# Kernel tuning notes

Hardware: AMD Instinct MI355X
Metric: run time of the kernel (lower is better)

Reference implementation:

```python
import jax, jax.numpy as jnp
import numpy as np

N_NODES = 50000
N_EDGES = 500000
D = 128  # input_dim == output_dim -> residual is identity


def _linear(x, W, b):
    return x @ W + b


def setup_inputs() -> dict:
    rng = np.random.default_rng(0)
    ei = rng.integers(0, N_NODES, size=(2, N_EDGES))
    # one-time structure cache: unique (src,dst) pairs + multiplicity counts
    pairs = np.stack([ei[0], ei[1]], axis=1)
    uniq, counts = np.unique(pairs, axis=0, return_counts=True)

    key = jax.random.key(0)
    ks = jax.random.split(key, 16)
    s = 0.02
    inp = {
        "x": jax.random.normal(ks[0], (N_NODES, D), jnp.float32),
        "src": jnp.asarray(uniq[:, 0], jnp.int32),
        "dst": jnp.asarray(uniq[:, 1], jnp.int32),
        "counts": jnp.asarray(counts, jnp.float32),
        # lin_src_to_dst / lin_dst_to_src (stored as [in, out])
        "W_sd": jax.random.normal(ks[1], (D, D), jnp.float32) * s,
        "b_sd": jnp.zeros((D,), jnp.float32),
        "W_ds": jax.random.normal(ks[2], (D, D), jnp.float32) * s,
        "b_ds": jnp.zeros((D,), jnp.float32),
        # lcs_mlp: Linear(2D, D) -> ReLU -> Linear(D, 1)
        "W_l1": jax.random.normal(ks[3], (2 * D, D), jnp.float32) * s,
        "b_l1": jnp.zeros((D,), jnp.float32),
        "W_l2": jax.random.normal(ks[4], (D, 1), jnp.float32) * s,
        "b_l2": jnp.zeros((1,), jnp.float32),
        # gate_mlp: Linear(2D, D) -> ReLU -> Linear(D, 1)
        "W_g1": jax.random.normal(ks[5], (2 * D, D), jnp.float32) * s,
        "b_g1": jnp.zeros((D,), jnp.float32),
        "W_g2": jax.random.normal(ks[6], (D, 1), jnp.float32) * s,
        "b_g2": jnp.zeros((1,), jnp.float32),
    }
    return inp


def reference(x, src, dst, counts, W_sd, b_sd, W_ds, b_ds,
              W_l1, b_l1, W_l2, b_l2, W_g1, b_g1, W_g2, b_g2):
    num_nodes = x.shape[0]
    x_src = x[src]                      # [E, D] gather
    x_dst = x[dst]                      # [E, D] gather

    # LCS score per unique edge (computed under no_grad in torch -> stop_gradient)
    lcs_in = jnp.concatenate([x_src, x_dst], axis=-1)           # [E, 2D]
    h = jax.nn.relu(_linear(lcs_in, W_l1, b_l1))
    lcs = jax.nn.sigmoid(_linear(h, W_l2, b_l2))                # [E, 1]
    lcs = jax.lax.stop_gradient(lcs)

    cnt = counts[:, None]                                       # [E, 1]
    msg_in = _linear(x_src, W_sd, b_sd) * lcs * cnt             # [E, D]
    msg_out = _linear(x_dst, W_ds, b_ds) * lcs * cnt            # [E, D]

    h_in = jax.ops.segment_sum(msg_in, dst, num_segments=num_nodes)
    h_out = jax.ops.segment_sum(msg_out, src, num_segments=num_nodes)

    in_deg = jnp.clip(jax.ops.segment_sum(counts, dst, num_segments=num_nodes), 1.0)
    out_deg = jnp.clip(jax.ops.segment_sum(counts, src, num_segments=num_nodes), 1.0)
    h_in = h_in / in_deg[:, None]
    h_out = h_out / out_deg[:, None]

    gate_in = jnp.concatenate([h_in, h_out], axis=-1)           # [N, 2D]
    g = jax.nn.relu(_linear(gate_in, W_g1, b_g1))
    gate = jax.nn.sigmoid(_linear(g, W_g2, b_g2))               # [N, 1]

    fused = gate * h_in + (1.0 - gate) * h_out
    return fused + x  # residual is Identity (input_dim == output_dim)
```

## Files before the change

### kernel.cpp

```cpp
#include <hip/hip_runtime.h>
#include <math.h>

typedef unsigned int uint;
typedef unsigned long long ull;

#define THREADS 256
#define NC 96

typedef __attribute__((ext_vector_type(8))) short bf16x8;
typedef __attribute__((ext_vector_type(4))) float f32x4;

__device__ __forceinline__ float blo(uint u) { return __uint_as_float(u << 16); }
__device__ __forceinline__ float bhi(uint u) { return __uint_as_float(u & 0xffff0000u); }
__device__ __forceinline__ uint  bf16r(float x) {
    uint u = __float_as_uint(x);
    return (u + 0x7fffu + ((u >> 16) & 1u)) >> 16;
}
__device__ __forceinline__ uint packbf(float lo, float hi) {
    return bf16r(lo) | (bf16r(hi) << 16);
}

__global__ __launch_bounds__(THREADS)
void transpose_w(const float* __restrict__ W_sd, const float* __restrict__ W_ds,
                 const float* __restrict__ W_l1, const float* __restrict__ W_g1,
                 ushort* __restrict__ Wt, ushort* __restrict__ Wtg1)
{
    __shared__ float tile[32][33];
    const int y = blockIdx.y;
    const float* src;
    ushort* dst;
    int dstK, kofs;
    if (y < 4) {
        src = (y == 0) ? W_sd : (y == 1) ? W_ds : (y == 2) ? W_l1 : (W_l1 + 16384);
        dst = Wt + y * 16384; dstK = 128; kofs = 0;
    } else {
        src = W_g1 + (y - 4) * 16384;
        dst = Wtg1; dstK = 256; kofs = (y - 4) * 128;
    }
    const int tix = blockIdx.x;
    const int k0 = (tix & 3) * 32, n0 = (tix >> 2) * 32;
    const int t = threadIdx.x;

    {
        const int r = t >> 3, c8 = t & 7;
        const float4 f = *(const float4*)(src + (size_t)(k0 + r) * 128 + n0 + c8 * 4);
        tile[r][c8 * 4 + 0] = f.x; tile[r][c8 * 4 + 1] = f.y;
        tile[r][c8 * 4 + 2] = f.z; tile[r][c8 * 4 + 3] = f.w;
    }
    __syncthreads();
    {
        const int n = t >> 3, k8 = t & 7;
        const float v0 = tile[k8 * 4 + 0][n], v1 = tile[k8 * 4 + 1][n];
        const float v2 = tile[k8 * 4 + 2][n], v3 = tile[k8 * 4 + 3][n];
        uint2 o; o.x = packbf(v0, v1); o.y = packbf(v2, v3);
        *(uint2*)(dst + (size_t)(n0 + n) * dstK + kofs + k0 + k8 * 4) = o;
    }
}

__device__ __forceinline__ void mfma_tile_compute(const char* AsB, const char* BtB,
                                                  int wv, int ln, f32x4 acc[8])
{
    const int mrow = wv * 16 + (ln & 15);
    const int kgb  = (ln >> 4) * 16;
#pragma unroll
    for (int kk = 0; kk < 4; ++kk) {
        const int kbyte = kk * 64 + kgb;
        const bf16x8 a = *(const bf16x8*)(AsB + mrow * 256 + (kbyte ^ ((mrow & 7) << 4)));
#pragma unroll
        for (int tt = 0; tt < 8; ++tt) {
            const int nrow = tt * 16 + (ln & 15);
            const bf16x8 b = *(const bf16x8*)(BtB + nrow * 256 + (kbyte ^ ((nrow & 7) << 4)));
            acc[tt] = __builtin_amdgcn_mfma_f32_16x16x32_bf16(a, b, acc[tt], 0, 0, 0);
        }
    }
}

__global__ __launch_bounds__(THREADS)
void gemm_node_count(const float* __restrict__ X, int M,
                     const ushort* __restrict__ Wt,
                     const float* __restrict__ b_sd, const float* __restrict__ b_ds,
                     const float* __restrict__ b_l1,
                     ushort* __restrict__ Pb,
                     const int* __restrict__ src, const int* __restrict__ dst,
                     const float* __restrict__ counts,
                     ull* __restrict__ packed_in, int* __restrict__ off_out,
                     int E, int ST, int BPG)
{
    __shared__ __align__(16) char BtB[32768];
    __shared__ __align__(16) char AsB[17408];

    const int tid = threadIdx.x;
    const int bid = blockIdx.x;

    if (bid < NC) {
        const int stride = NC * THREADS;
        for (int e = bid * THREADS + tid; e < E; e += stride) {
            const int  d = dst[e];
            const uint c = (uint)counts[e];
            atomicAdd(packed_in + d, (1ULL << 32) | (ull)c);
        }
        for (int e = bid * THREADS + tid; e < E; e += stride) {
            const int cur  = src[e];
            const int prev = (e == 0) ? -1 : src[e - 1];
            for (int v = prev + 1; v <= cur; ++v) off_out[v] = e;
            if (e == E - 1)
                for (int v = cur + 1; v <= M; ++v) off_out[v] = E;
        }
        return;
    }

    const int q    = bid - NC;
    const int grp  = q & 3;
    const int sidx = q >> 2;
    const int wv = tid >> 6, ln = tid & 63;
    const int r = tid >> 2, seg = tid & 3;

    if (sidx * 4 >= ST) return;

    {
        const int rn = tid >> 1, sg = tid & 1;
        const uint4* ws = (const uint4*)(Wt + grp * 16384 + (size_t)rn * 128 + sg * 64);
#pragma unroll
        for (int i = 0; i < 8; ++i) {
            const uint4 u = ws[i];
            const int kbyte = sg * 128 + i * 16;
            *(uint4*)(BtB + rn * 256 + (kbyte ^ ((rn & 7) << 4))) = u;
        }
    }

    const float* bias = (grp == 0) ? b_sd : (grp == 1) ? b_ds
                      : (grp == 2) ? b_l1 : nullptr;
    float bv[8];
#pragma unroll
    for (int tt = 0; tt < 8; ++tt)
        bv[tt] = bias ? bias[tt * 16 + (ln & 15)] : 0.f;

    float4 fa[8];
    {
        int gr = sidx * 4 * 64 + r; if (gr >= M) gr = M - 1;
        const float4* xs = (const float4*)(X + (size_t)gr * 128 + seg * 32);
#pragma unroll
        for (int i = 0; i < 8; ++i) fa[i] = xs[i];
    }

    for (int k = 0; k < 4; ++k) {
        const int s = sidx * 4 + k;
        if (s >= ST) break;
        __syncthreads();

#pragma unroll
        for (int i = 0; i < 4; ++i) {
            const float4 f0 = fa[i * 2], f1 = fa[i * 2 + 1];
            uint4 u;
            u.x = packbf(f0.x, f0.y); u.y = packbf(f0.z, f0.w);
            u.z = packbf(f1.x, f1.y); u.w = packbf(f1.z, f1.w);
            const int kbyte = seg * 64 + i * 16;
            *(uint4*)(AsB + r * 256 + (kbyte ^ ((r & 7) << 4))) = u;
        }
        __syncthreads();

        if (k < 3 && s + 1 < ST) {
            int gr = (s + 1) * 64 + r; if (gr >= M) gr = M - 1;
            const float4* xs = (const float4*)(X + (size_t)gr * 128 + seg * 32);
#pragma unroll
            for (int i = 0; i < 8; ++i) fa[i] = xs[i];
        }

        f32x4 acc[8];
#pragma unroll
        for (int tt = 0; tt < 8; ++tt) acc[tt] = (f32x4){0.f, 0.f, 0.f, 0.f};
        mfma_tile_compute(AsB, BtB, wv, ln, acc);
        __syncthreads();

#pragma unroll
        for (int tt = 0; tt < 8; ++tt) {
            const int n = tt * 16 + (ln & 15);
#pragma unroll
            for (int r2 = 0; r2 < 4; ++r2) {
                const int m = wv * 16 + ((ln >> 4) << 2) + r2;
                ((ushort*)AsB)[m * 136 + n] = (ushort)bf16r(acc[tt][r2] + bv[tt]);
            }
        }
        __syncthreads();

        {
            const int gr = s * 64 + r;
            if (gr < M) {
                uint4* dstp = (uint4*)Pb + (size_t)gr * 64 + grp * 16 + seg * 4;
#pragma unroll
                for (int i = 0; i < 4; ++i)
                    dstp[i] = *(const uint4*)(AsB + r * 272 + (seg * 4 + i) * 16);
            }
        }
    }
}

__global__ __launch_bounds__(256)
void scan_p1(const ull* __restrict__ packed_in, int* __restrict__ bsum, int M)
{
    __shared__ int s[256];
    const int t = threadIdx.x;
    const int i = blockIdx.x * 256 + t;
    s[t] = (i < M) ? (int)(packed_in[i] >> 32) : 0;
    __syncthreads();
#pragma unroll
    for (int o = 128; o; o >>= 1) {
        if (t < o) s[t] += s[t + o];
        __syncthreads();
    }
    if (t == 0) bsum[blockIdx.x] = s[0];
}

__global__ __launch_bounds__(1024)
void scan_p2(int* __restrict__ bsum, int NB)
{
    __shared__ int s[1024];
    const int t = threadIdx.x;
    const int v = (t < NB) ? bsum[t] : 0;
    s[t] = v;
    __syncthreads();
    for (int o = 1; o < 1024; o <<= 1) {
        const int u = (t >= o) ? s[t - o] : 0;
        __syncthreads();
        s[t] += u;
        __syncthreads();
    }
    if (t < NB) bsum[t] = s[t] - v;
}

__global__ __launch_bounds__(256)
void scan_p3(const ull* __restrict__ packed_in, const int* __restrict__ bsum,
             int* __restrict__ off_in, int M)
{
    __shared__ int s[256];
    const int t = threadIdx.x;
    const int i = blockIdx.x * 256 + t;
    const int v = (i < M) ? (int)(packed_in[i] >> 32) : 0;
    s[t] = v;
    __syncthreads();
    for (int o = 1; o < 256; o <<= 1) {
        const int u = (t >= o) ? s[t - o] : 0;
        __syncthreads();
        s[t] += u;
        __syncthreads();
    }
    if (i < M) off_in[i] = bsum[blockIdx.x] + s[t] - v;
}

__global__ __launch_bounds__(THREADS)
void edge_out(const ushort* __restrict__ Pb, ushort* __restrict__ Hout,
              const int* __restrict__ dst, const float* __restrict__ counts,
              const float* __restrict__ W_l2, const float* __restrict__ b_l2,
              const int* __restrict__ off_out,
              const int* __restrict__ off_in, int* __restrict__ cur_in,
              float2* __restrict__ uw_in, int M)
{
    const int lane = threadIdx.x & 63;
    const int wid  = threadIdx.x >> 6;
    const int v    = blockIdx.x * 4 + wid;
    if (v >= M) return;
    const int g  = lane >> 4;
    const int gl = lane & 15;

    const uint* rs = (const uint*)Pb + (size_t)v * 256;
    const uint4 av = ((const uint4*)(rs + 128))[gl];
    const float4 wa = ((const float4*)W_l2)[gl * 2];
    const float4 wb = ((const float4*)W_l2)[gl * 2 + 1];
    const float bl2 = b_l2[0];

    const int base = off_out[v];
    const int end  = off_out[v + 1];

    float a0 = 0.f, a1 = 0.f, a2 = 0.f, a3 = 0.f;
    float a4 = 0.f, a5 = 0.f, a6 = 0.f, a7 = 0.f;
    float dg = 0.f;

    int j = base + g;
    int   d0 = 0;  float c0 = 0.f;
    uint4 bv0 = {0, 0, 0, 0}, pv0 = {0, 0, 0, 0};
    if (j < end) {
        d0 = dst[j]; c0 = counts[j];
        const uint* rd = (const uint*)Pb + (size_t)d0 * 256;
        bv0 = ((const uint4*)(rd + 192))[gl];
        pv0 = ((const uint4*)(rd + 64))[gl];
    }

    for (; j < end; j += 4) {
        const int jn = j + 4;
        const int jc = (jn < end) ? jn : j;
        const int   d1 = dst[jc];
        const float c1 = counts[jc];
        const uint* rdn = (const uint*)Pb + (size_t)d1 * 256;
        const uint4 bv1 = ((const uint4*)(rdn + 192))[gl];
        const uint4 pv1 = ((const uint4*)(rdn + 64))[gl];

        float part =
            fmaxf(blo(av.x) + blo(bv0.x), 0.f) * wa.x + fmaxf(bhi(av.x) + bhi(bv0.x), 0.f) * wa.y +
            fmaxf(blo(av.y) + blo(bv0.y), 0.f) * wa.z + fmaxf(bhi(av.y) + bhi(bv0.y), 0.f) * wa.w +
            fmaxf(blo(av.z) + blo(bv0.z), 0.f) * wb.x + fmaxf(bhi(av.z) + bhi(bv0.z), 0.f) * wb.y +
            fmaxf(blo(av.w) + blo(bv0.w), 0.f) * wb.z + fmaxf(bhi(av.w) + bhi(bv0.w), 0.f) * wb.w;
        part += __shfl_xor(part, 1);
        part += __shfl_xor(part, 2);
        part += __shfl_xor(part, 4);
        part += __shfl_xor(part, 8);

        const float w = c0 / (1.f + __expf(-(part + bl2)));

        a0 = fmaf(blo(pv0.x), w, a0); a1 = fmaf(bhi(pv0.x), w, a1);
        a2 = fmaf(blo(pv0.y), w, a2); a3 = fmaf(bhi(pv0.y), w, a3);
        a4 = fmaf(blo(pv0.z), w, a4); a5 = fmaf(bhi(pv0.z), w, a5);
        a6 = fmaf(blo(pv0.w), w, a6); a7 = fmaf(bhi(pv0.w), w, a7);
        dg += c0;

        if (gl == 0) {
            const int r1 = atomicAdd(cur_in + d0, 1);
            uw_in[off_in[d0] + r1] = make_float2(__int_as_float(v), w);
        }

        d0 = d1; c0 = c1; bv0 = bv1; pv0 = pv1;
    }

#define RED2(a) a += __shfl_xor(a, 16); a += __shfl_xor(a, 32);
    RED2(a0) RED2(a1) RED2(a2) RED2(a3) RED2(a4) RED2(a5) RED2(a6) RED2(a7) RED2(dg)
#undef RED2

    if (g == 0) {
        const float r = 1.f / fmaxf(dg, 1.f);
        uint4 o;
        o.x = packbf(a0 * r, a1 * r);
        o.y = packbf(a2 * r, a3 * r);
        o.z = packbf(a4 * r, a5 * r);
        o.w = packbf(a6 * r, a7 * r);
        ((uint4*)((uint*)Hout + (size_t)v * 64))[gl] = o;
    }
}

__global__ __launch_bounds__(THREADS)
void agg_in(ushort* __restrict__ Pb,
            const float2* __restrict__ uw_in,
            const int* __restrict__ off_in, const ull* __restrict__ packed_in,
            int M)
{
    const int lane = threadIdx.x & 63;
    const int wid  = threadIdx.x >> 6;
    const int v    = blockIdx.x * 4 + wid;
    if (v >= M) return;
    const int g  = lane >> 4;
    const int gl = lane & 15;

    const ull pk = packed_in[v];
    const int n  = (int)(pk >> 32);
    const float dg = (float)(uint)(pk & 0xffffffffu);
    const float2* __restrict__ uw = uw_in + off_in[v];

    float a0 = 0.f, a1 = 0.f, a2 = 0.f, a3 = 0.f;
    float a4 = 0.f, a5 = 0.f, a6 = 0.f, a7 = 0.f;

    int j = g;
    float2 p0 = make_float2(0.f, 0.f);
    uint4  pv0 = {0, 0, 0, 0};
    if (j < n) {
        p0 = uw[j];
        pv0 = ((const uint4*)((const uint*)Pb + (size_t)__float_as_int(p0.x) * 256))[gl];
    }

    for (; j < n; j += 4) {
        const int jn = j + 4;
        const int jc = (jn < n) ? jn : j;
        const float2 p1 = uw[jc];
        const uint4  pv1 = ((const uint4*)((const uint*)Pb + (size_t)__float_as_int(p1.x) * 256))[gl];

        const float w = p0.y;
        a0 = fmaf(blo(pv0.x), w, a0); a1 = fmaf(bhi(pv0.x), w, a1);
        a2 = fmaf(blo(pv0.y), w, a2); a3 = fmaf(bhi(pv0.y), w, a3);
        a4 = fmaf(blo(pv0.z), w, a4); a5 = fmaf(bhi(pv0.z), w, a5);
        a6 = fmaf(blo(pv0.w), w, a6); a7 = fmaf(bhi(pv0.w), w, a7);

        p0 = p1; pv0 = pv1;
    }
#define RED2(a) a += __shfl_xor(a, 16); a += __shfl_xor(a, 32);
    RED2(a0) RED2(a1) RED2(a2) RED2(a3) RED2(a4) RED2(a5) RED2(a6) RED2(a7)
#undef RED2

    if (g == 0) {
        const float r = 1.f / fmaxf(dg, 1.f);
        uint4 o;
        o.x = packbf(a0 * r, a1 * r);
        o.y = packbf(a2 * r, a3 * r);
        o.z = packbf(a4 * r, a5 * r);
        o.w = packbf(a6 * r, a7 * r);
        ((uint4*)((uint*)Pb + (size_t)v * 256 + 128))[gl] = o;
    }
}

__global__ __launch_bounds__(THREADS)
void gate_final(const ushort* __restrict__ Pb, const ushort* __restrict__ Hout,
                int M,
                const ushort* __restrict__ Wtg1, const float* __restrict__ b_g1,
                const float* __restrict__ W_g2, const float* __restrict__ b_g2,
                const float* __restrict__ x, float* __restrict__ out)
{
    __shared__ __align__(16) char AsB[16384];
    __shared__ __align__(16) char BtB[32768];

    const int tid = threadIdx.x;
    const int m0  = blockIdx.x * 64;
    const int wv = tid >> 6, ln = tid & 63;

    f32x4 acc[8];
#pragma unroll
    for (int tt = 0; tt < 8; ++tt) acc[tt] = (f32x4){0.f, 0.f, 0.f, 0.f};

    for (int h = 0; h < 2; ++h) {
        if (h) __syncthreads();
        {
            const int r = tid >> 2, seg = tid & 3;
            int gr = m0 + r; if (gr >= M) gr = M - 1;
            const uint4* ps = (h == 0)
                ? ((const uint4*)Pb + (size_t)gr * 64 + 32 + seg * 4)
                : ((const uint4*)Hout + (size_t)gr * 16 + seg * 4);
#pragma unroll
            for (int i = 0; i < 4; ++i) {
                const uint4 u = ps[i];
                const int kbyte = seg * 64 + i * 16;
                *(uint4*)(AsB + r * 256 + (kbyte ^ ((r & 7) << 4))) = u;
            }
        }
        {
            const int rn = tid >> 1, sg = tid & 1;
            const uint4* ws = (const uint4*)Wtg1 + (size_t)rn * 32 + h * 16 + sg * 8;
#pragma unroll
            for (int i = 0; i < 8; ++i) {
                const uint4 u = ws[i];
                const int kbyte = sg * 128 + i * 16;
                *(uint4*)(BtB + rn * 256 + (kbyte ^ ((rn & 7) << 4))) = u;
            }
        }
        __syncthreads();
        mfma_tile_compute(AsB, BtB, wv, ln, acc);
    }

    __syncthreads();
#pragma unroll
    for (int tt = 0; tt < 8; ++tt) {
        const int n = tt * 16 + (ln & 15);
        const float bv = b_g1[n];
#pragma unroll
        for (int r = 0; r < 4; ++r) {
            const int m = wv * 16 + ((ln >> 4) << 2) + r;
            const float val = fmaxf(acc[tt][r] + bv, 0.f);
            const float pr  = __shfl_xor(val, 1);
            if ((ln & 1) == 0)
                ((uint*)BtB)[m * 68 + (n >> 1)] = packbf(val, pr);
        }
    }
    __syncthreads();

    const float bg2 = b_g2[0];
    const float2 w2 = ((const float2*)W_g2)[ln];
#pragma unroll 4
    for (int r = 0; r < 16; ++r) {
        const int row = wv * 16 + r;
        const int gr  = m0 + row;
        const uint gv = ((const uint*)BtB)[row * 68 + ln];
        float part = blo(gv) * w2.x + bhi(gv) * w2.y;
#pragma unroll
        for (int off = 32; off; off >>= 1) part += __shfl_xor(part, off);
        const float gate = 1.f / (1.f + __expf(-(part + bg2)));
        if (gr < M) {
            const uint hin = ((const uint*)Pb)[(size_t)gr * 256 + 128 + ln];
            const uint hov = ((const uint*)Hout)[(size_t)gr * 64 + ln];
            const float2 xv = ((const float2*)x)[(size_t)gr * 64 + ln];
            float2 o;
            o.x = gate * blo(hin) + (1.f - gate) * blo(hov) + xv.x;
            o.y = gate * bhi(hin) + (1.f - gate) * bhi(hov) + xv.y;
            ((float2*)out)[(size_t)gr * 64 + ln] = o;
        }
    }
}

extern "C" void kernel_launch(void* const* d_in, const int* in_sizes, int n_in,
                              void* d_out, int out_size, void* d_ws, size_t ws_size,
                              hipStream_t stream)
{
    const float* x     = (const float*)d_in[0];
    const int*   src   = (const int*)  d_in[1];
    const int*   dst   = (const int*)  d_in[2];
    const float* cnts  = (const float*)d_in[3];
    const float* W_sd  = (const float*)d_in[4];
    const float* b_sd  = (const float*)d_in[5];
    const float* W_ds  = (const float*)d_in[6];
    const float* b_ds  = (const float*)d_in[7];
    const float* W_l1  = (const float*)d_in[8];
    const float* b_l1  = (const float*)d_in[9];
    const float* W_l2  = (const float*)d_in[10];
    const float* b_l2  = (const float*)d_in[11];
    const float* W_g1  = (const float*)d_in[12];
    const float* b_g1  = (const float*)d_in[13];
    const float* W_g2  = (const float*)d_in[14];
    const float* b_g2  = (const float*)d_in[15];

    const int M = in_sizes[0] / 128;
    const int E = in_sizes[1];

    ushort* Pb        = (ushort*)d_ws;
    ushort* Wt        = Pb + (size_t)M * 512;
    ushort* Wtg1      = Wt + 4 * 16384;
    ushort* Hout      = Wtg1 + 32768;
    ull*    packed_in = (ull*)(Hout + (size_t)M * 128);
    int*    cur_in    = (int*)(packed_in + M);
    float2* uw_in     = (float2*)(cur_in + M);
    int*    off_in    = (int*)(uw_in + E);
    int*    off_out   = off_in + M;
    int*    bsum      = off_out + M + 1;

    hipMemsetAsync(packed_in, 0, 12 * (size_t)M, stream);

    transpose_w<<<dim3(16, 6), THREADS, 0, stream>>>(W_sd, W_ds, W_l1, W_g1, Wt, Wtg1);

    const int ST  = (M + 63) / 64;
    const int BPG = (ST + 3) / 4;
    gemm_node_count<<<NC + 4 * BPG, THREADS, 0, stream>>>(
        x, M, Wt, b_sd, b_ds, b_l1, Pb, src, dst, cnts, packed_in, off_out,
        E, ST, BPG);

    const int NB = (M + 255) / 256;
    scan_p1<<<NB, 256, 0, stream>>>(packed_in, bsum, M);
    scan_p2<<<1, 1024, 0, stream>>>(bsum, NB);
    scan_p3<<<NB, 256, 0, stream>>>(packed_in, bsum, off_in, M);

    edge_out<<<(M + 3) / 4, THREADS, 0, stream>>>(
        Pb, Hout, dst, cnts, W_l2, b_l2, off_out, off_in, cur_in, uw_in, M);

    agg_in<<<(M + 3) / 4, THREADS, 0, stream>>>(Pb, uw_in, off_in, packed_in, M);

    gate_final<<<(M + 63) / 64, THREADS, 0, stream>>>(Pb, Hout, M, Wtg1, b_g1,
                                                      W_g2, b_g2, x, (float*)d_out);
}
```

Before: 182.2 us.

## Load GEMM A operand directly into registers and remap blocks across XCDs

The node GEMM now loads X rows straight into MFMA A-fragment registers instead of staging them through shared memory, which removes several barriers and the LDS A buffer. Results are written directly from accumulators as packed bf16 pairs via lane shuffles instead of an LDS transpose and coalesced uint4 stores. Block indices are also permuted so that consecutive work items are spread across the eight XCDs, with the grid padded to a multiple of 8. The trade is less LDS traffic and synchronisation against uncoalesced 4-byte global stores and strided global loads of X.

```diff
diff --git a/kernel.cpp b/kernel.cpp
--- a/kernel.cpp
+++ b/kernel.cpp
@@ -57,24 +57,6 @@
     }
 }
 
-__device__ __forceinline__ void mfma_tile_compute(const char* AsB, const char* BtB,
-                                                  int wv, int ln, f32x4 acc[8])
-{
-    const int mrow = wv * 16 + (ln & 15);
-    const int kgb  = (ln >> 4) * 16;
-#pragma unroll
-    for (int kk = 0; kk < 4; ++kk) {
-        const int kbyte = kk * 64 + kgb;
-        const bf16x8 a = *(const bf16x8*)(AsB + mrow * 256 + (kbyte ^ ((mrow & 7) << 4)));
-#pragma unroll
-        for (int tt = 0; tt < 8; ++tt) {
-            const int nrow = tt * 16 + (ln & 15);
-            const bf16x8 b = *(const bf16x8*)(BtB + nrow * 256 + (kbyte ^ ((nrow & 7) << 4)));
-            acc[tt] = __builtin_amdgcn_mfma_f32_16x16x32_bf16(a, b, acc[tt], 0, 0, 0);
-        }
-    }
-}
-
 __global__ __launch_bounds__(THREADS)
 void gemm_node_count(const float* __restrict__ X, int M,
                      const ushort* __restrict__ Wt,
@@ -84,10 +66,9 @@
                      const int* __restrict__ src, const int* __restrict__ dst,
                      const float* __restrict__ counts,
                      ull* __restrict__ packed_in, int* __restrict__ off_out,
-                     int E, int ST, int BPG)
+                     int E, int ST, int NG)
 {
     __shared__ __align__(16) char BtB[32768];
-    __shared__ __align__(16) char AsB[17408];
 
     const int tid = threadIdx.x;
     const int bid = blockIdx.x;
@@ -109,13 +90,15 @@
         return;
     }
 
-    const int q    = bid - NC;
-    const int grp  = q & 3;
-    const int sidx = q >> 2;
+    const int bg   = bid - NC;
+    const int per  = NG >> 3;
+    const int p    = (bg & 7) * per + (bg >> 3);
+    if (p >= NG) return;
+    const int grp  = p & 3;
+    const int sidx = p >> 2;
+    if (sidx * 4 >= ST) return;
+
     const int wv = tid >> 6, ln = tid & 63;
-    const int r = tid >> 2, seg = tid & 3;
-
-    if (sidx * 4 >= ST) return;
 
     {
         const int rn = tid >> 1, sg = tid & 1;
@@ -127,6 +110,7 @@
             *(uint4*)(BtB + rn * 256 + (kbyte ^ ((rn & 7) << 4))) = u;
         }
     }
+    __syncthreads();
 
     const float* bias = (grp == 0) ? b_sd : (grp == 1) ? b_ds
                       : (grp == 2) ? b_l1 : nullptr;
@@ -135,61 +119,72 @@
     for (int tt = 0; tt < 8; ++tt)
         bv[tt] = bias ? bias[tt * 16 + (ln & 15)] : 0.f;
 
-    float4 fa[8];
+    const int rowA = wv * 16 + (ln & 15);
+    const int kofs = (ln >> 4) * 8;
+
+    float4 raw[8];
     {
-        int gr = sidx * 4 * 64 + r; if (gr >= M) gr = M - 1;
-        const float4* xs = (const float4*)(X + (size_t)gr * 128 + seg * 32);
-#pragma unroll
-        for (int i = 0; i < 8; ++i) fa[i] = xs[i];
+        int gr = sidx * 4 * 64 + rowA; if (gr >= M) gr = M - 1;
+        const float* xr = X + (size_t)gr * 128 + kofs;
+#pragma unroll
+        for (int kk = 0; kk < 4; ++kk) {
+            raw[2 * kk]     = *(const float4*)(xr + kk * 32);
+            raw[2 * kk + 1] = *(const float4*)(xr + kk * 32 + 4);
+        }
     }
 
     for (int k = 0; k < 4; ++k) {
         const int s = sidx * 4 + k;
         if (s >= ST) break;
-        __syncthreads();
-
-#pragma unroll
-        for (int i = 0; i < 4; ++i) {
-            const float4 f0 = fa[i * 2], f1 = fa[i * 2 + 1];
+
+        bf16x8 af[4];
+#pragma unroll
+        for (int kk = 0; kk < 4; ++kk) {
             uint4 u;
-            u.x = packbf(f0.x, f0.y); u.y = packbf(f0.z, f0.w);
-            u.z = packbf(f1.x, f1.y); u.w = packbf(f1.z, f1.w);
-            const int kbyte = seg * 64 + i * 16;
-            *(uint4*)(AsB + r * 256 + (kbyte ^ ((r & 7) << 4))) = u;
-        }
-        __syncthreads();
+            u.x = packbf(raw[2 * kk].x, raw[2 * kk].y);
+            u.y = packbf(raw[2 * kk].z, raw[2 * kk].w);
+            u.z = packbf(raw[2 * kk + 1].x, raw[2 * kk + 1].y);
+            u.w = packbf(raw[2 * kk + 1].z, raw[2 * kk + 1].w);
+            af[kk] = *reinterpret_cast<bf16x8*>(&u);
+        }
 
         if (k < 3 && s + 1 < ST) {
-            int gr = (s + 1) * 64 + r; if (gr >= M) gr = M - 1;
-            const float4* xs = (const float4*)(X + (size_t)gr * 128 + seg * 32);
-#pragma unroll
-            for (int i = 0; i < 8; ++i) fa[i] = xs[i];
+            int gr = (s + 1) * 64 + rowA; if (gr >= M) gr = M - 1;
+            const float* xr = X + (size_t)gr * 128 + kofs;
+#pragma unroll
+            for (int kk = 0; kk < 4; ++kk) {
+                raw[2 * kk]     = *(const float4*)(xr + kk * 32);
+                raw[2 * kk + 1] = *(const float4*)(xr + kk * 32 + 4);
+            }
         }
 
         f32x4 acc[8];
 #pragma unroll
         for (int tt = 0; tt < 8; ++tt) acc[tt] = (f32x4){0.f, 0.f, 0.f, 0.f};
-        mfma_tile_compute(AsB, BtB, wv, ln, acc);
-        __syncthreads();
+        const int kgb = (ln >> 4) * 16;
+#pragma unroll
+        for (int kk = 0; kk < 4; ++kk) {
+            const int kbyte = kk * 64 + kgb;
+#pragma unroll
+            for (int tt = 0; tt < 8; ++tt) {
+                const int nrow = tt * 16 + (ln & 15);
+                const bf16x8 b = *(const bf16x8*)(BtB + nrow * 256 + (kbyte ^ ((nrow & 7) << 4)));
+                acc[tt] = __builtin_amdgcn_mfma_f32_16x16x32_bf16(af[kk], b, acc[tt], 0, 0, 0);
+            }
+        }
 
 #pragma unroll
         for (int tt = 0; tt < 8; ++tt) {
-            const int n = tt * 16 + (ln & 15);
 #pragma unroll
             for (int r2 = 0; r2 < 4; ++r2) {
-                const int m = wv * 16 + ((ln >> 4) << 2) + r2;
-                ((ushort*)AsB)[m * 136 + n] = (ushort)bf16r(acc[tt][r2] + bv[tt]);
-            }
-        }
-        __syncthreads();
-
-        {
-            const int gr = s * 64 + r;
-            if (gr < M) {
-                uint4* dstp = (uint4*)Pb + (size_t)gr * 64 + grp * 16 + seg * 4;
-#pragma unroll
-                for (int i = 0; i < 4; ++i)
-                    dstp[i] = *(const uint4*)(AsB + r * 272 + (seg * 4 + i) * 16);
+                const float val = acc[tt][r2] + bv[tt];
+                const float pr  = __shfl_xor(val, 1);
+                const int gr = s * 64 + wv * 16 + ((ln >> 4) << 2) + r2;
+                if ((ln & 1) == 0 && gr < M) {
+                    uint* dstp = (uint*)Pb + (size_t)gr * 256 + grp * 64
+                               + tt * 8 + ((ln & 15) >> 1);
+                    *dstp = packbf(val, pr);
+                }
             }
         }
     }
@@ -411,6 +406,7 @@
 #pragma unroll
     for (int tt = 0; tt < 8; ++tt) acc[tt] = (f32x4){0.f, 0.f, 0.f, 0.f};
 
+    const int kgb = (ln >> 4) * 16;
     for (int h = 0; h < 2; ++h) {
         if (h) __syncthreads();
         {
@@ -437,7 +433,20 @@
             }
         }
         __syncthreads();
-        mfma_tile_compute(AsB, BtB, wv, ln, acc);
+        {
+            const int mrow = wv * 16 + (ln & 15);
+#pragma unroll
+            for (int kk = 0; kk < 4; ++kk) {
+                const int kbyte = kk * 64 + kgb;
+                const bf16x8 a = *(const bf16x8*)(AsB + mrow * 256 + (kbyte ^ ((mrow & 7) << 4)));
+#pragma unroll
+                for (int tt = 0; tt < 8; ++tt) {
+                    const int nrow = tt * 16 + (ln & 15);
+                    const bf16x8 b = *(const bf16x8*)(BtB + nrow * 256 + (kbyte ^ ((nrow & 7) << 4)));
+                    acc[tt] = __builtin_amdgcn_mfma_f32_16x16x32_bf16(a, b, acc[tt], 0, 0, 0);
+                }
+            }
+        }
     }
 
     __syncthreads();
@@ -520,9 +529,11 @@
 
     const int ST  = (M + 63) / 64;
     const int BPG = (ST + 3) / 4;
-    gemm_node_count<<<NC + 4 * BPG, THREADS, 0, stream>>>(
+    int NG = 4 * BPG;
+    NG = ((NG + 7) / 8) * 8;
+    gemm_node_count<<<NC + NG, THREADS, 0, stream>>>(
         x, M, Wt, b_sd, b_ds, b_l1, Pb, src, dst, cnts, packed_in, off_out,
-        E, ST, BPG);
+        E, ST, NG);
 
     const int NB = (M + 255) / 256;
     scan_p1<<<NB, 256, 0, stream>>>(packed_in, bsum, M);
```

Result: no change. 179.0 us (-1.8%).
